# Kernel optimization log

Measured on AMD Instinct MI355X. Metric: run time of the kernel, lower is better.

The kernel has to match this reference:

```python
import jax, jax.numpy as jnp
import numpy as np

B, S, D, H = 2, 2048, 1024, 16
HD = D // H  # head dim = 64


def setup_inputs() -> dict:
    key = jax.random.key(0)
    ks = jax.random.split(key, 9)
    std = 0.02
    return {
        "hidden_states": jax.random.normal(ks[0], (B, S, D), jnp.float32),
        "wq": jax.random.normal(ks[1], (D, D), jnp.float32) * std,
        "bq": jnp.zeros((D,), jnp.float32),
        "wk": jax.random.normal(ks[2], (D, D), jnp.float32) * std,
        "bk": jnp.zeros((D,), jnp.float32),
        "wv": jax.random.normal(ks[3], (D, D), jnp.float32) * std,
        "bv": jnp.zeros((D,), jnp.float32),
        "wo": jax.random.normal(ks[4], (D, D), jnp.float32) * std,
        "bo": jnp.zeros((D,), jnp.float32),
    }


def reference(hidden_states, wq, bq, wk, bk, wv, bv, wo, bo):
    b, s, d = hidden_states.shape
    # projections (torch Linear: x @ W.T + b; here weights stored as [in,out]-equivalent transpose)
    q = hidden_states @ wq.T + bq
    k = hidden_states @ wk.T + bk
    v = hidden_states @ wv.T + bv
    # [b, h, s, hd]
    q = q.reshape(b, s, H, HD).transpose(0, 2, 1, 3)
    k = k.reshape(b, s, H, HD).transpose(0, 2, 1, 3)
    v = v.reshape(b, s, H, HD).transpose(0, 2, 1, 3)
    scores = jnp.einsum("bhqd,bhkd->bhqk", q, k) / jnp.sqrt(jnp.float32(HD))
    probs = jax.nn.softmax(scores, axis=-1)  # dropout p=0 (eval)
    ctx = jnp.einsum("bhqk,bhkd->bhqd", probs, v)
    ctx = ctx.transpose(0, 2, 1, 3).reshape(b, s, d)
    return ctx @ wo.T + bo
```

## Files before the change

### kernel.cpp

```cpp
#include <hip/hip_runtime.h>
#include <math.h>
#include <stdint.h>

constexpr int BB  = 2;
constexpr int SS  = 2048;
constexpr int DD  = 1024;
constexpr int HH  = 16;
constexpr int HDD = 64;
constexpr int MM  = BB * SS;

typedef uint16_t u16;
typedef __attribute__((ext_vector_type(4))) float    f32x4;
typedef __attribute__((ext_vector_type(8))) _Float16 f16x8;
typedef __attribute__((ext_vector_type(4))) _Float16 f16x4;
typedef __attribute__((ext_vector_type(8))) short    s16x8;
typedef __attribute__((ext_vector_type(4))) unsigned int u32x4;

__device__ __forceinline__ u16 to_f16(float f) {
    const _Float16 h = (_Float16)f;
    return __builtin_bit_cast(u16, h);
}

__device__ __forceinline__ f32x4 mfma32(s16x8 a, s16x8 b, f32x4 c) {
    return __builtin_amdgcn_mfma_f32_16x16x32_f16(
        __builtin_bit_cast(f16x8, a), __builtin_bit_cast(f16x8, b), c, 0, 0, 0);
}
__device__ __forceinline__ f32x4 mfma32_ff(s16x8 a, f16x8 b, f32x4 c) {
    return __builtin_amdgcn_mfma_f32_16x16x32_f16(
        __builtin_bit_cast(f16x8, a), b, c, 0, 0, 0);
}

__device__ __forceinline__ void load_lds16(const void* g, void* l) {
    __builtin_amdgcn_global_load_lds(
        (const __attribute__((address_space(1))) void*)g,
        (__attribute__((address_space(3))) void*)l, 16, 0, 0);
}

__global__ __launch_bounds__(256) void cast_all(
    const float* __restrict__ x,
    const float* __restrict__ w0, const float* __restrict__ w1,
    const float* __restrict__ w2, const float* __restrict__ w3,
    u16* __restrict__ xb, u16* __restrict__ wb)
{
    const int blk = blockIdx.x, tid = threadIdx.x;
    const float* src; u16* dst; int idx;
    if (blk < 2048) { src = x; dst = xb; idx = blk * 256 + tid; }
    else {
        const int b2 = blk - 2048, which = b2 >> 9;
        src = (which == 0) ? w0 : (which == 1) ? w1 : (which == 2) ? w2 : w3;
        dst = wb + ((size_t)which << 20);
        idx = (b2 & 511) * 256 + tid;
    }
    const float4* in4 = (const float4*)src;
    const float4 a = in4[idx * 2], b = in4[idx * 2 + 1];
    s16x8 v;
    v[0] = (short)to_f16(a.x); v[1] = (short)to_f16(a.y);
    v[2] = (short)to_f16(a.z); v[3] = (short)to_f16(a.w);
    v[4] = (short)to_f16(b.x); v[5] = (short)to_f16(b.y);
    v[6] = (short)to_f16(b.z); v[7] = (short)to_f16(b.w);
    *(s16x8*)(dst + (size_t)idx * 8) = v;
}

template <bool SWAP>
__device__ __forceinline__ void kloop64(
    const u16* __restrict__ Ag, const u16* __restrict__ Wg,
    u16* Abase, u16* Bbase, const int w4,
    const int lane, const int wm, const int wn, f32x4 (&acc)[4][4])
{
    const int lt = lane & 15, quad = lane >> 4;
    const int cb = w4 * 4;

#define STG64(buf_, ko_) do {                                              \
    _Pragma("unroll")                                                      \
    for (int c = 0; c < 4; ++c) {                                          \
        load_lds16(Ag + (size_t)((cb + c) * 8) * 1024 + (ko_),             \
                   Abase + (buf_) * 8192 + (cb + c) * 512);                \
        load_lds16(Wg + (size_t)((cb + c) * 8) * 1024 + (ko_),             \
                   Bbase + (buf_) * 8192 + (cb + c) * 512);                \
    } } while (0)

    STG64(0, 0);

#pragma unroll 1
    for (int it = 0; it < 8; ++it) {
        const int buf = it & 1;
        __syncthreads();
        if (it < 7) STG64(buf ^ 1, (it + 1) * 64);
        const u16* Acur = Abase + buf * 8192;
        const u16* Bcur = Bbase + buf * 8192;

        s16x8 af[2][4], bf[2][4];
#pragma unroll
        for (int kk = 0; kk < 2; ++kk) {
#pragma unroll
            for (int i = 0; i < 4; ++i) {
                const int row = wm + i * 16 + lt;
                af[kk][i] = *(const s16x8*)(Acur + row * 64 +
                                (((kk * 4 + quad) ^ (row & 7)) * 8));
            }
#pragma unroll
            for (int j = 0; j < 4; ++j) {
                const int row = wn + j * 16 + lt;
                bf[kk][j] = *(const s16x8*)(Bcur + row * 64 +
                                (((kk * 4 + quad) ^ (row & 7)) * 8));
            }
        }
#pragma unroll
        for (int i = 0; i < 4; ++i)
#pragma unroll
            for (int j = 0; j < 4; ++j) {
                if (SWAP) {
                    acc[i][j] = mfma32(bf[0][j], af[0][i], acc[i][j]);
                    acc[i][j] = mfma32(bf[1][j], af[1][i], acc[i][j]);
                } else {
                    acc[i][j] = mfma32(af[0][i], bf[0][j], acc[i][j]);
                    acc[i][j] = mfma32(af[1][i], bf[1][j], acc[i][j]);
                }
            }
    }
#undef STG64
}

template <int MODE>
__global__ __launch_bounds__(512) void gemm_mfma(
    const u16* __restrict__ A, const u16* __restrict__ Wb,
    const float* __restrict__ b0, const float* __restrict__ b1,
    const float* __restrict__ b2,
    float* __restrict__ outf, u16* __restrict__ outq, u16* __restrict__ outv)
{
    __shared__ u16 smem[65536];

    const int tid = threadIdx.x, lane = tid & 63, wid = tid >> 6;
    const int grp = wid >> 2, w4 = wid & 3;
    const int quad = lane >> 4;

    const int bm = blockIdx.y * 128;
    const int nb = blockIdx.x * 128;
    const int which = nb >> 10;
    const int ncol  = nb & 1023;
    const u16* Wblk = Wb + ((size_t)which << 20) + (size_t)ncol * 1024;

    const int rbase = lane >> 3;
    const int gu    = (lane & 7) ^ rbase;
    const u16* Ag = A    + (size_t)(bm + rbase) * 1024 + grp * 512 + gu * 8;
    const u16* Wg = Wblk + (size_t)rbase        * 1024 + grp * 512 + gu * 8;
    u16* Abase = smem + grp * 16384;
    u16* Bbase = smem + 32768 + grp * 16384;

    f32x4 acc[4][4];
#pragma unroll
    for (int i = 0; i < 4; ++i)
#pragma unroll
        for (int j = 0; j < 4; ++j) { f32x4 z = {0.f, 0.f, 0.f, 0.f}; acc[i][j] = z; }

    const int wm = (w4 >> 1) * 64, wn = (w4 & 1) * 64;
    const bool swap = (MODE == 0) || (which < 2);
    if (swap) kloop64<true >(Ag, Wg, Abase, Bbase, w4, lane, wm, wn, acc);
    else      kloop64<false>(Ag, Wg, Abase, Bbase, w4, lane, wm, wn, acc);

    __syncthreads();
    float* rp = (float*)smem;
    const int slot = (w4 * 64 + lane) * 4;
    if (grp == 1) {
#pragma unroll
        for (int i = 0; i < 4; ++i)
#pragma unroll
            for (int j = 0; j < 4; ++j)
                *(f32x4*)(rp + (i * 4 + j) * 1024 + slot) = acc[i][j];
    }
    __syncthreads();
    if (grp != 0) return;
#pragma unroll
    for (int i = 0; i < 4; ++i)
#pragma unroll
        for (int j = 0; j < 4; ++j)
            acc[i][j] += *(const f32x4*)(rp + (i * 4 + j) * 1024 + slot);

    if (MODE == 0) {
#pragma unroll
        for (int j = 0; j < 4; ++j) {
            const int n0 = nb + wn + 16 * j + quad * 4;
            const float4 bv = *(const float4*)&b0[n0];
#pragma unroll
            for (int i = 0; i < 4; ++i) {
                const int m = bm + wm + 16 * i + (lane & 15);
                f32x4 w = acc[i][j];
                w[0] += bv.x; w[1] += bv.y; w[2] += bv.z; w[3] += bv.w;
                *(f32x4*)&outf[(size_t)m * 1024 + n0] = w;
            }
        }
    } else if (which < 2) {
        const float* bias = which ? b1 : b0;
        const float scale = which ? 1.0f : 0.125f;
        u16* outb = outq + ((size_t)which << 22);
        const int h = (ncol + wn) >> 6;
#pragma unroll
        for (int j = 0; j < 4; ++j) {
            const int nl0 = ncol + wn + 16 * j + quad * 4;
            const float4 bv = *(const float4*)&bias[nl0];
            const int hd0 = 16 * j + quad * 4;
#pragma unroll
            for (int i = 0; i < 4; ++i) {
                const int m = bm + wm + 16 * i + (lane & 15);
                const int b_ = m >> 11, s = m & 2047;
                f16x4 w;
                w[0] = (_Float16)((acc[i][j][0] + bv.x) * scale);
                w[1] = (_Float16)((acc[i][j][1] + bv.y) * scale);
                w[2] = (_Float16)((acc[i][j][2] + bv.z) * scale);
                w[3] = (_Float16)((acc[i][j][3] + bv.w) * scale);
                *(f16x4*)&outb[(((size_t)(b_ * HH + h)) * SS + s) * HDD + hd0] = w;
            }
        }
    } else {
        const int kt = ((bm + wm) & 2047) >> 6;
        const int b_ = (bm + wm) >> 11;
#pragma unroll
        for (int j = 0; j < 4; ++j) {
            const int nl = ncol + wn + 16 * j + (lane & 15);
            const float bb = b2[nl];
            const int h = nl >> 6, hd = nl & 63;
            u16* vrow = outv + (((size_t)(b_ * HH + h)) * HDD + hd) * SS + kt * 64;
#pragma unroll
            for (int i = 0; i < 4; ++i) {
                const int p0 = (i >> 1) * 32 + quad * 8 + (i & 1) * 4;
                f16x4 w;
                w[0] = (_Float16)(acc[i][j][0] + bb);
                w[1] = (_Float16)(acc[i][j][1] + bb);
                w[2] = (_Float16)(acc[i][j][2] + bb);
                w[3] = (_Float16)(acc[i][j][3] + bb);
                *(f16x4*)&vrow[p0] = w;
            }
        }
    }
}

__global__ __launch_bounds__(512, 4) void attn_mfma(
    const u16* __restrict__ Q, const u16* __restrict__ Kg,
    const u16* __restrict__ Vt, u16* __restrict__ ctx)
{
    __shared__ u16 smem[32768];

    const int tid = threadIdx.x, lane = tid & 63, wid = tid >> 6;
    const int grp = wid >> 2, w4 = wid & 3;
    const int quad = lane >> 4;

    const int orig   = blockIdx.y * 16 + blockIdx.x;
    const int xcd    = orig & 7, within = orig >> 3;
    const int bh     = xcd * 4 + (within >> 4);
    const int q0     = (within & 15) * 128;

    const u16* Qb = Q  + (size_t)bh * SS * HDD;
    const u16* Kb = Kg + (size_t)bh * SS * HDD + (size_t)grp * 1024 * HDD;
    const u16* Vb = Vt + (size_t)bh * HDD * SS + grp * 1024;

    u16* Kbase = smem + grp * 8192;
    u16* Vbase = smem + 16384 + grp * 8192;

    const int qa = q0 + w4 * 32 + (lane & 15);
    const s16x8 bq0a = *(const s16x8*)(Qb + (size_t)qa * HDD + quad * 8);
    const s16x8 bq1a = *(const s16x8*)(Qb + (size_t)qa * HDD + 32 + quad * 8);
    const s16x8 bq0b = *(const s16x8*)(Qb + (size_t)(qa + 16) * HDD + quad * 8);
    const s16x8 bq1b = *(const s16x8*)(Qb + (size_t)(qa + 16) * HDD + 32 + quad * 8);

    f32x4 oa[4], ob[4];
    f32x4 la4 = {0.f, 0.f, 0.f, 0.f}, lb4 = {0.f, 0.f, 0.f, 0.f};
#pragma unroll
    for (int m = 0; m < 4; ++m) {
        f32x4 z = {0.f, 0.f, 0.f, 0.f};
        oa[m] = z; ob[m] = z;
    }
    const s16x8 ones = {15360, 15360, 15360, 15360,
                        15360, 15360, 15360, 15360};

    const int c0 = w4 * 2, c1 = c0 + 1;
    const int r0 = (c0 * 64 + lane) >> 3, lu0 = ((lane & 7) ^ (r0 & 7));
    const int r1 = (c1 * 64 + lane) >> 3, lu1 = ((lane & 7) ^ (r1 & 7));
    const u16* Kp0 = Kb + (size_t)r0 * HDD + lu0 * 8;
    const u16* Kp1 = Kb + (size_t)r1 * HDD + lu1 * 8;
    const u16* Vp0 = Vb + (size_t)r0 * SS + lu0 * 8;
    const u16* Vp1 = Vb + (size_t)r1 * SS + lu1 * 8;

    load_lds16(Kp0, Kbase + c0 * 512);
    load_lds16(Kp1, Kbase + c1 * 512);
    load_lds16(Vp0, Vbase + c0 * 512);
    load_lds16(Vp1, Vbase + c1 * 512);

    for (int kt = 0; kt < 16; ++kt) {
        const int buf = kt & 1;
        __syncthreads();

        if (kt + 1 < 16) {
            const int nb_ = (buf ^ 1) * 4096;
            load_lds16(Kp0 + (size_t)(kt + 1) * 64 * HDD, Kbase + nb_ + c0 * 512);
            load_lds16(Kp1 + (size_t)(kt + 1) * 64 * HDD, Kbase + nb_ + c1 * 512);
            load_lds16(Vp0 + (kt + 1) * 64, Vbase + nb_ + c0 * 512);
            load_lds16(Vp1 + (kt + 1) * 64, Vbase + nb_ + c1 * 512);
        }
        const u16* Kbuf = Kbase + buf * 4096;
        const u16* Vbuf = Vbase + buf * 4096;

        f32x4 Sa[4], Sb[4];
#pragma unroll
        for (int j = 0; j < 4; ++j) {
            const int row = j * 16 + (lane & 15);
            const int sw = lane & 7;
            const s16x8 ak0 = *(const s16x8*)(Kbuf + (size_t)row * 64 + ((quad    ) ^ sw) * 8);
            const s16x8 ak1 = *(const s16x8*)(Kbuf + (size_t)row * 64 + ((quad + 4) ^ sw) * 8);
            f32x4 za = {0.f, 0.f, 0.f, 0.f};
            za = mfma32(ak0, bq0a, za);
            za = mfma32(ak1, bq1a, za);
            Sa[j] = za;
            f32x4 zb = {0.f, 0.f, 0.f, 0.f};
            zb = mfma32(ak0, bq0b, zb);
            zb = mfma32(ak1, bq1b, zb);
            Sb[j] = zb;
        }

        f16x8 pb0a, pb1a, pb0b, pb1b;
        {
            u32x4 u;
            u[0] = __builtin_bit_cast(unsigned int, __builtin_amdgcn_cvt_pkrtz(__expf(Sa[0][0]), __expf(Sa[0][1])));
            u[1] = __builtin_bit_cast(unsigned int, __builtin_amdgcn_cvt_pkrtz(__expf(Sa[0][2]), __expf(Sa[0][3])));
            u[2] = __builtin_bit_cast(unsigned int, __builtin_amdgcn_cvt_pkrtz(__expf(Sa[1][0]), __expf(Sa[1][1])));
            u[3] = __builtin_bit_cast(unsigned int, __builtin_amdgcn_cvt_pkrtz(__expf(Sa[1][2]), __expf(Sa[1][3])));
            pb0a = __builtin_bit_cast(f16x8, u);
            u[0] = __builtin_bit_cast(unsigned int, __builtin_amdgcn_cvt_pkrtz(__expf(Sa[2][0]), __expf(Sa[2][1])));
            u[1] = __builtin_bit_cast(unsigned int, __builtin_amdgcn_cvt_pkrtz(__expf(Sa[2][2]), __expf(Sa[2][3])));
            u[2] = __builtin_bit_cast(unsigned int, __builtin_amdgcn_cvt_pkrtz(__expf(Sa[3][0]), __expf(Sa[3][1])));
            u[3] = __builtin_bit_cast(unsigned int, __builtin_amdgcn_cvt_pkrtz(__expf(Sa[3][2]), __expf(Sa[3][3])));
            pb1a = __builtin_bit_cast(f16x8, u);
            u[0] = __builtin_bit_cast(unsigned int, __builtin_amdgcn_cvt_pkrtz(__expf(Sb[0][0]), __expf(Sb[0][1])));
            u[1] = __builtin_bit_cast(unsigned int, __builtin_amdgcn_cvt_pkrtz(__expf(Sb[0][2]), __expf(Sb[0][3])));
            u[2] = __builtin_bit_cast(unsigned int, __builtin_amdgcn_cvt_pkrtz(__expf(Sb[1][0]), __expf(Sb[1][1])));
            u[3] = __builtin_bit_cast(unsigned int, __builtin_amdgcn_cvt_pkrtz(__expf(Sb[1][2]), __expf(Sb[1][3])));
            pb0b = __builtin_bit_cast(f16x8, u);
            u[0] = __builtin_bit_cast(unsigned int, __builtin_amdgcn_cvt_pkrtz(__expf(Sb[2][0]), __expf(Sb[2][1])));
            u[1] = __builtin_bit_cast(unsigned int, __builtin_amdgcn_cvt_pkrtz(__expf(Sb[2][2]), __expf(Sb[2][3])));
            u[2] = __builtin_bit_cast(unsigned int, __builtin_amdgcn_cvt_pkrtz(__expf(Sb[3][0]), __expf(Sb[3][1])));
            u[3] = __builtin_bit_cast(unsigned int, __builtin_amdgcn_cvt_pkrtz(__expf(Sb[3][2]), __expf(Sb[3][3])));
            pb1b = __builtin_bit_cast(f16x8, u);
        }

        la4 = mfma32_ff(ones, pb0a, la4);
        la4 = mfma32_ff(ones, pb1a, la4);
        lb4 = mfma32_ff(ones, pb0b, lb4);
        lb4 = mfma32_ff(ones, pb1b, lb4);

#pragma unroll
        for (int m = 0; m < 4; ++m) {
            const int row = m * 16 + (lane & 15);
            const int sw = lane & 7;
            const s16x8 v0 = *(const s16x8*)(Vbuf + (size_t)row * 64 + ((quad    ) ^ sw) * 8);
            const s16x8 v1 = *(const s16x8*)(Vbuf + (size_t)row * 64 + ((quad + 4) ^ sw) * 8);
            oa[m] = mfma32_ff(v0, pb0a, oa[m]);
            oa[m] = mfma32_ff(v1, pb1a, oa[m]);
            ob[m] = mfma32_ff(v0, pb0b, ob[m]);
            ob[m] = mfma32_ff(v1, pb1b, ob[m]);
        }
    }

    __syncthreads();
    float* ep = (float*)smem;
    float* lp = ep + 8 * 1088;
    if (grp == 1) {
#pragma unroll
        for (int sub = 0; sub < 2; ++sub) {
            const float* src = (sub == 0) ? (const float*)&oa[0] : (const float*)&ob[0];
            float* base = ep + (w4 * 2 + sub) * 1088 + (lane & 15) * 68 + quad * 4;
#pragma unroll
            for (int m = 0; m < 4; ++m)
                *(f32x4*)(base + m * 16) = *(const f32x4*)(src + m * 4);
        }
        if (quad == 0) {
            lp[(w4 * 2 + 0) * 16 + (lane & 15)] = la4[0];
            lp[(w4 * 2 + 1) * 16 + (lane & 15)] = lb4[0];
        }
    }
    __syncthreads();
    if (grp == 0) {
        const int b_ = bh >> 4, h = bh & 15;
#pragma unroll
        for (int sub = 0; sub < 2; ++sub) {
            const f32x4* own = (sub == 0) ? &oa[0] : &ob[0];
            const float lown = (sub == 0) ? la4[0] : lb4[0];
            const float inv = 1.f / (lown + lp[(w4 * 2 + sub) * 16 + (lane & 15)]);
            const float* base = ep + (w4 * 2 + sub) * 1088 + (lane & 15) * 68 + quad * 4;
            const int s_idx = q0 + w4 * 32 + sub * 16 + (lane & 15);
            u16* orow = ctx + ((size_t)(b_ * SS + s_idx)) * DD + h * HDD;
#pragma unroll
            for (int m = 0; m < 4; ++m) {
                const f32x4 part = *(const f32x4*)(base + m * 16);
                f16x4 w;
#pragma unroll
                for (int r = 0; r < 4; ++r)
                    w[r] = (_Float16)((own[m][r] + part[r]) * inv);
                *(f16x4*)(orow + m * 16 + quad * 4) = w;
            }
        }
    }
}

extern "C" void kernel_launch(void* const* d_in, const int* in_sizes, int n_in,
                              void* d_out, int out_size, void* d_ws, size_t ws_size,
                              hipStream_t stream)
{
    const float* x  = (const float*)d_in[0];
    const float* wq = (const float*)d_in[1];
    const float* bq = (const float*)d_in[2];
    const float* wk = (const float*)d_in[3];
    const float* bk = (const float*)d_in[4];
    const float* wv = (const float*)d_in[5];
    const float* bv = (const float*)d_in[6];
    const float* wo = (const float*)d_in[7];
    const float* bo = (const float*)d_in[8];

    u16* xb   = (u16*)d_ws;
    u16* wb   = xb  + ((size_t)4  << 20);
    u16* qk   = wb  + ((size_t)4  << 20);
    u16* vtw  = qk  + ((size_t)8  << 20);
    u16* ctxb = vtw + ((size_t)4  << 20);

    cast_all<<<4096, 256, 0, stream>>>(x, wq, wk, wv, wo, xb, wb);

    gemm_mfma<1><<<dim3(24, 32), 512, 0, stream>>>(
        xb, wb, bq, bk, bv, nullptr, qk, vtw);

    attn_mfma<<<dim3(16, 32), 512, 0, stream>>>(
        qk, qk + ((size_t)4 << 20), vtw, ctxb);

    gemm_mfma<0><<<dim3(8, 32), 512, 0, stream>>>(
        ctxb, wb + ((size_t)3 << 20), bo, nullptr, nullptr,
        (float*)d_out, nullptr, nullptr);
}
```

Baseline: 183.7 us.

## Software-pipeline attention loop: overlap QK of next tile with PV of previous

Restructures the key-tile loop so that each iteration computes QK scores and exp for tile kt while doing the PV accumulation for tile kt-1. This lets the matrix and exp work of two stages interleave instead of running back to back. V tiles move to a three-slot ring buffer in LDS so the previous tile's V stays valid while the next one loads, which raises the block's LDS use from 64KB to 80KB. Holding both the previous and the new P fragments in registers raises register pressure, and the loop is no longer unrolled.

```diff
diff --git a/kernel.cpp b/kernel.cpp
--- a/kernel.cpp
+++ b/kernel.cpp
@@ -238,7 +238,7 @@
     const u16* __restrict__ Q, const u16* __restrict__ Kg,
     const u16* __restrict__ Vt, u16* __restrict__ ctx)
 {
-    __shared__ u16 smem[32768];
+    __shared__ u16 smem[40960];
 
     const int tid = threadIdx.x, lane = tid & 63, wid = tid >> 6;
     const int grp = wid >> 2, w4 = wid & 3;
@@ -254,7 +254,7 @@
     const u16* Vb = Vt + (size_t)bh * HDD * SS + grp * 1024;
 
     u16* Kbase = smem + grp * 8192;
-    u16* Vbase = smem + 16384 + grp * 8192;
+    u16* Vbase = smem + 16384 + grp * 12288;
 
     const int qa = q0 + w4 * 32 + (lane & 15);
     const s16x8 bq0a = *(const s16x8*)(Qb + (size_t)qa * HDD + quad * 8);
@@ -280,26 +280,10 @@
     const u16* Vp0 = Vb + (size_t)r0 * SS + lu0 * 8;
     const u16* Vp1 = Vb + (size_t)r1 * SS + lu1 * 8;
 
-    load_lds16(Kp0, Kbase + c0 * 512);
-    load_lds16(Kp1, Kbase + c1 * 512);
-    load_lds16(Vp0, Vbase + c0 * 512);
-    load_lds16(Vp1, Vbase + c1 * 512);
-
-    for (int kt = 0; kt < 16; ++kt) {
-        const int buf = kt & 1;
-        __syncthreads();
-
-        if (kt + 1 < 16) {
-            const int nb_ = (buf ^ 1) * 4096;
-            load_lds16(Kp0 + (size_t)(kt + 1) * 64 * HDD, Kbase + nb_ + c0 * 512);
-            load_lds16(Kp1 + (size_t)(kt + 1) * 64 * HDD, Kbase + nb_ + c1 * 512);
-            load_lds16(Vp0 + (kt + 1) * 64, Vbase + nb_ + c0 * 512);
-            load_lds16(Vp1 + (kt + 1) * 64, Vbase + nb_ + c1 * 512);
-        }
-        const u16* Kbuf = Kbase + buf * 4096;
-        const u16* Vbuf = Vbase + buf * 4096;
-
-        f32x4 Sa[4], Sb[4];
+    f16x8 pA0, pA1, pB0, pB1;
+
+    f32x4 Sa[4], Sb[4];
+    auto qk_tiles = [&](const u16* Kbuf) {
 #pragma unroll
         for (int j = 0; j < 4; ++j) {
             const int row = j * 16 + (lane & 15);
@@ -315,49 +299,73 @@
             zb = mfma32(ak1, bq1b, zb);
             Sb[j] = zb;
         }
-
-        f16x8 pb0a, pb1a, pb0b, pb1b;
-        {
-            u32x4 u;
-            u[0] = __builtin_bit_cast(unsigned int, __builtin_amdgcn_cvt_pkrtz(__expf(Sa[0][0]), __expf(Sa[0][1])));
-            u[1] = __builtin_bit_cast(unsigned int, __builtin_amdgcn_cvt_pkrtz(__expf(Sa[0][2]), __expf(Sa[0][3])));
-            u[2] = __builtin_bit_cast(unsigned int, __builtin_amdgcn_cvt_pkrtz(__expf(Sa[1][0]), __expf(Sa[1][1])));
-            u[3] = __builtin_bit_cast(unsigned int, __builtin_amdgcn_cvt_pkrtz(__expf(Sa[1][2]), __expf(Sa[1][3])));
-            pb0a = __builtin_bit_cast(f16x8, u);
-            u[0] = __builtin_bit_cast(unsigned int, __builtin_amdgcn_cvt_pkrtz(__expf(Sa[2][0]), __expf(Sa[2][1])));
-            u[1] = __builtin_bit_cast(unsigned int, __builtin_amdgcn_cvt_pkrtz(__expf(Sa[2][2]), __expf(Sa[2][3])));
-            u[2] = __builtin_bit_cast(unsigned int, __builtin_amdgcn_cvt_pkrtz(__expf(Sa[3][0]), __expf(Sa[3][1])));
-            u[3] = __builtin_bit_cast(unsigned int, __builtin_amdgcn_cvt_pkrtz(__expf(Sa[3][2]), __expf(Sa[3][3])));
-            pb1a = __builtin_bit_cast(f16x8, u);
-            u[0] = __builtin_bit_cast(unsigned int, __builtin_amdgcn_cvt_pkrtz(__expf(Sb[0][0]), __expf(Sb[0][1])));
-            u[1] = __builtin_bit_cast(unsigned int, __builtin_amdgcn_cvt_pkrtz(__expf(Sb[0][2]), __expf(Sb[0][3])));
-            u[2] = __builtin_bit_cast(unsigned int, __builtin_amdgcn_cvt_pkrtz(__expf(Sb[1][0]), __expf(Sb[1][1])));
-            u[3] = __builtin_bit_cast(unsigned int, __builtin_amdgcn_cvt_pkrtz(__expf(Sb[1][2]), __expf(Sb[1][3])));
-            pb0b = __builtin_bit_cast(f16x8, u);
-            u[0] = __builtin_bit_cast(unsigned int, __builtin_amdgcn_cvt_pkrtz(__expf(Sb[2][0]), __expf(Sb[2][1])));
-            u[1] = __builtin_bit_cast(unsigned int, __builtin_amdgcn_cvt_pkrtz(__expf(Sb[2][2]), __expf(Sb[2][3])));
-            u[2] = __builtin_bit_cast(unsigned int, __builtin_amdgcn_cvt_pkrtz(__expf(Sb[3][0]), __expf(Sb[3][1])));
-            u[3] = __builtin_bit_cast(unsigned int, __builtin_amdgcn_cvt_pkrtz(__expf(Sb[3][2]), __expf(Sb[3][3])));
-            pb1b = __builtin_bit_cast(f16x8, u);
-        }
-
-        la4 = mfma32_ff(ones, pb0a, la4);
-        la4 = mfma32_ff(ones, pb1a, la4);
-        lb4 = mfma32_ff(ones, pb0b, lb4);
-        lb4 = mfma32_ff(ones, pb1b, lb4);
-
+    };
+    auto exp_pack = [&](const f32x4* S, f16x8& o0, f16x8& o1) {
+        u32x4 u;
+        u[0] = __builtin_bit_cast(unsigned int, __builtin_amdgcn_cvt_pkrtz(__expf(S[0][0]), __expf(S[0][1])));
+        u[1] = __builtin_bit_cast(unsigned int, __builtin_amdgcn_cvt_pkrtz(__expf(S[0][2]), __expf(S[0][3])));
+        u[2] = __builtin_bit_cast(unsigned int, __builtin_amdgcn_cvt_pkrtz(__expf(S[1][0]), __expf(S[1][1])));
+        u[3] = __builtin_bit_cast(unsigned int, __builtin_amdgcn_cvt_pkrtz(__expf(S[1][2]), __expf(S[1][3])));
+        o0 = __builtin_bit_cast(f16x8, u);
+        u[0] = __builtin_bit_cast(unsigned int, __builtin_amdgcn_cvt_pkrtz(__expf(S[2][0]), __expf(S[2][1])));
+        u[1] = __builtin_bit_cast(unsigned int, __builtin_amdgcn_cvt_pkrtz(__expf(S[2][2]), __expf(S[2][3])));
+        u[2] = __builtin_bit_cast(unsigned int, __builtin_amdgcn_cvt_pkrtz(__expf(S[3][0]), __expf(S[3][1])));
+        u[3] = __builtin_bit_cast(unsigned int, __builtin_amdgcn_cvt_pkrtz(__expf(S[3][2]), __expf(S[3][3])));
+        o1 = __builtin_bit_cast(f16x8, u);
+    };
+    auto do_pv = [&](const u16* Vbuf) {
+        la4 = mfma32_ff(ones, pA0, la4);
+        la4 = mfma32_ff(ones, pA1, la4);
+        lb4 = mfma32_ff(ones, pB0, lb4);
+        lb4 = mfma32_ff(ones, pB1, lb4);
 #pragma unroll
         for (int m = 0; m < 4; ++m) {
             const int row = m * 16 + (lane & 15);
             const int sw = lane & 7;
             const s16x8 v0 = *(const s16x8*)(Vbuf + (size_t)row * 64 + ((quad    ) ^ sw) * 8);
             const s16x8 v1 = *(const s16x8*)(Vbuf + (size_t)row * 64 + ((quad + 4) ^ sw) * 8);
-            oa[m] = mfma32_ff(v0, pb0a, oa[m]);
-            oa[m] = mfma32_ff(v1, pb1a, oa[m]);
-            ob[m] = mfma32_ff(v0, pb0b, ob[m]);
-            ob[m] = mfma32_ff(v1, pb1b, ob[m]);
-        }
-    }
+            oa[m] = mfma32_ff(v0, pA0, oa[m]);
+            oa[m] = mfma32_ff(v1, pA1, oa[m]);
+            ob[m] = mfma32_ff(v0, pB0, ob[m]);
+            ob[m] = mfma32_ff(v1, pB1, ob[m]);
+        }
+    };
+
+    load_lds16(Kp0, Kbase + c0 * 512);
+    load_lds16(Kp1, Kbase + c1 * 512);
+    load_lds16(Vp0, Vbase + c0 * 512);
+    load_lds16(Vp1, Vbase + c1 * 512);
+
+    __syncthreads();
+    load_lds16(Kp0 + 64 * HDD, Kbase + 4096 + c0 * 512);
+    load_lds16(Kp1 + 64 * HDD, Kbase + 4096 + c1 * 512);
+    load_lds16(Vp0 + 64,       Vbase + 4096 + c0 * 512);
+    load_lds16(Vp1 + 64,       Vbase + 4096 + c1 * 512);
+    qk_tiles(Kbase);
+    exp_pack(Sa, pA0, pA1);
+    exp_pack(Sb, pB0, pB1);
+
+    int sl_prev = 0, sl_next = 2;
+#pragma unroll 1
+    for (int kt = 1; kt < 16; ++kt) {
+        const int kb = kt & 1;
+        __syncthreads();
+        if (kt < 15) {
+            load_lds16(Kp0 + (size_t)(kt + 1) * 64 * HDD, Kbase + (kb ^ 1) * 4096 + c0 * 512);
+            load_lds16(Kp1 + (size_t)(kt + 1) * 64 * HDD, Kbase + (kb ^ 1) * 4096 + c1 * 512);
+            load_lds16(Vp0 + (kt + 1) * 64, Vbase + sl_next * 4096 + c0 * 512);
+            load_lds16(Vp1 + (kt + 1) * 64, Vbase + sl_next * 4096 + c1 * 512);
+        }
+        qk_tiles(Kbase + kb * 4096);
+        f16x8 nA0, nA1, nB0, nB1;
+        exp_pack(Sa, nA0, nA1);
+        exp_pack(Sb, nB0, nB1);
+        do_pv(Vbase + sl_prev * 4096);
+        pA0 = nA0; pA1 = nA1; pB0 = nB0; pB1 = nB1;
+        sl_prev = (sl_prev == 2) ? 0 : sl_prev + 1;
+        sl_next = (sl_next == 2) ? 0 : sl_next + 1;
+    }
+    do_pv(Vbase);
 
     __syncthreads();
     float* ep = (float*)smem;
```

Result: slower. 189.5 us (+3.2%).

## Process 64 query rows per wave in attention to reuse K/V tiles

Applied to the files above, without the earlier changes.

Each wave in the attention kernel now handles four 16-row query sub-tiles instead of two, so a block covers 256 queries and the grid halves. Each K and V fragment read from LDS feeds twice as many MFMAs, and each block reloads K/V half as often across the sequence. The cost is more accumulator registers, so launch bounds drop to 2 blocks per CU and the epilogue scratch grows. Fewer blocks and lower occupancy may leave CUs underused.

```diff
diff --git a/kernel.cpp b/kernel.cpp
--- a/kernel.cpp
+++ b/kernel.cpp
@@ -234,20 +234,20 @@
     }
 }
 
-__global__ __launch_bounds__(512, 4) void attn_mfma(
+__global__ __launch_bounds__(512, 2) void attn_mfma(
     const u16* __restrict__ Q, const u16* __restrict__ Kg,
     const u16* __restrict__ Vt, u16* __restrict__ ctx)
 {
-    __shared__ u16 smem[32768];
+    __shared__ u16 smem[35840];
 
     const int tid = threadIdx.x, lane = tid & 63, wid = tid >> 6;
     const int grp = wid >> 2, w4 = wid & 3;
-    const int quad = lane >> 4;
-
-    const int orig   = blockIdx.y * 16 + blockIdx.x;
+    const int quad = lane >> 4, lt = lane & 15, sw = lane & 7;
+
+    const int orig   = blockIdx.y * 8 + blockIdx.x;
     const int xcd    = orig & 7, within = orig >> 3;
-    const int bh     = xcd * 4 + (within >> 4);
-    const int q0     = (within & 15) * 128;
+    const int bh     = xcd * 4 + (within >> 3);
+    const int q0     = (within & 7) * 256;
 
     const u16* Qb = Q  + (size_t)bh * SS * HDD;
     const u16* Kb = Kg + (size_t)bh * SS * HDD + (size_t)grp * 1024 * HDD;
@@ -256,18 +256,22 @@
     u16* Kbase = smem + grp * 8192;
     u16* Vbase = smem + 16384 + grp * 8192;
 
-    const int qa = q0 + w4 * 32 + (lane & 15);
-    const s16x8 bq0a = *(const s16x8*)(Qb + (size_t)qa * HDD + quad * 8);
-    const s16x8 bq1a = *(const s16x8*)(Qb + (size_t)qa * HDD + 32 + quad * 8);
-    const s16x8 bq0b = *(const s16x8*)(Qb + (size_t)(qa + 16) * HDD + quad * 8);
-    const s16x8 bq1b = *(const s16x8*)(Qb + (size_t)(qa + 16) * HDD + 32 + quad * 8);
-
-    f32x4 oa[4], ob[4];
-    f32x4 la4 = {0.f, 0.f, 0.f, 0.f}, lb4 = {0.f, 0.f, 0.f, 0.f};
-#pragma unroll
-    for (int m = 0; m < 4; ++m) {
+    const int qa = q0 + w4 * 64 + lt;
+    s16x8 bq[4][2];
+#pragma unroll
+    for (int s = 0; s < 4; ++s) {
+        bq[s][0] = *(const s16x8*)(Qb + (size_t)(qa + 16 * s) * HDD + quad * 8);
+        bq[s][1] = *(const s16x8*)(Qb + (size_t)(qa + 16 * s) * HDD + 32 + quad * 8);
+    }
+
+    f32x4 o[4][4];
+    f32x4 l4[4];
+#pragma unroll
+    for (int s = 0; s < 4; ++s) {
         f32x4 z = {0.f, 0.f, 0.f, 0.f};
-        oa[m] = z; ob[m] = z;
+        l4[s] = z;
+#pragma unroll
+        for (int m = 0; m < 4; ++m) o[s][m] = z;
     }
     const s16x8 ones = {15360, 15360, 15360, 15360,
                         15360, 15360, 15360, 15360};
@@ -285,6 +289,7 @@
     load_lds16(Vp0, Vbase + c0 * 512);
     load_lds16(Vp1, Vbase + c1 * 512);
 
+#pragma unroll 1
     for (int kt = 0; kt < 16; ++kt) {
         const int buf = kt & 1;
         __syncthreads();
@@ -299,93 +304,78 @@
         const u16* Kbuf = Kbase + buf * 4096;
         const u16* Vbuf = Vbase + buf * 4096;
 
-        f32x4 Sa[4], Sb[4];
-#pragma unroll
-        for (int j = 0; j < 4; ++j) {
-            const int row = j * 16 + (lane & 15);
-            const int sw = lane & 7;
-            const s16x8 ak0 = *(const s16x8*)(Kbuf + (size_t)row * 64 + ((quad    ) ^ sw) * 8);
-            const s16x8 ak1 = *(const s16x8*)(Kbuf + (size_t)row * 64 + ((quad + 4) ^ sw) * 8);
-            f32x4 za = {0.f, 0.f, 0.f, 0.f};
-            za = mfma32(ak0, bq0a, za);
-            za = mfma32(ak1, bq1a, za);
-            Sa[j] = za;
-            f32x4 zb = {0.f, 0.f, 0.f, 0.f};
-            zb = mfma32(ak0, bq0b, zb);
-            zb = mfma32(ak1, bq1b, zb);
-            Sb[j] = zb;
-        }
-
-        f16x8 pb0a, pb1a, pb0b, pb1b;
-        {
-            u32x4 u;
-            u[0] = __builtin_bit_cast(unsigned int, __builtin_amdgcn_cvt_pkrtz(__expf(Sa[0][0]), __expf(Sa[0][1])));
-            u[1] = __builtin_bit_cast(unsigned int, __builtin_amdgcn_cvt_pkrtz(__expf(Sa[0][2]), __expf(Sa[0][3])));
-            u[2] = __builtin_bit_cast(unsigned int, __builtin_amdgcn_cvt_pkrtz(__expf(Sa[1][0]), __expf(Sa[1][1])));
-            u[3] = __builtin_bit_cast(unsigned int, __builtin_amdgcn_cvt_pkrtz(__expf(Sa[1][2]), __expf(Sa[1][3])));
-            pb0a = __builtin_bit_cast(f16x8, u);
-            u[0] = __builtin_bit_cast(unsigned int, __builtin_amdgcn_cvt_pkrtz(__expf(Sa[2][0]), __expf(Sa[2][1])));
-            u[1] = __builtin_bit_cast(unsigned int, __builtin_amdgcn_cvt_pkrtz(__expf(Sa[2][2]), __expf(Sa[2][3])));
-            u[2] = __builtin_bit_cast(unsigned int, __builtin_amdgcn_cvt_pkrtz(__expf(Sa[3][0]), __expf(Sa[3][1])));
-            u[3] = __builtin_bit_cast(unsigned int, __builtin_amdgcn_cvt_pkrtz(__expf(Sa[3][2]), __expf(Sa[3][3])));
-            pb1a = __builtin_bit_cast(f16x8, u);
-            u[0] = __builtin_bit_cast(unsigned int, __builtin_amdgcn_cvt_pkrtz(__expf(Sb[0][0]), __expf(Sb[0][1])));
-            u[1] = __builtin_bit_cast(unsigned int, __builtin_amdgcn_cvt_pkrtz(__expf(Sb[0][2]), __expf(Sb[0][3])));
-            u[2] = __builtin_bit_cast(unsigned int, __builtin_amdgcn_cvt_pkrtz(__expf(Sb[1][0]), __expf(Sb[1][1])));
-            u[3] = __builtin_bit_cast(unsigned int, __builtin_amdgcn_cvt_pkrtz(__expf(Sb[1][2]), __expf(Sb[1][3])));
-            pb0b = __builtin_bit_cast(f16x8, u);
-            u[0] = __builtin_bit_cast(unsigned int, __builtin_amdgcn_cvt_pkrtz(__expf(Sb[2][0]), __expf(Sb[2][1])));
-            u[1] = __builtin_bit_cast(unsigned int, __builtin_amdgcn_cvt_pkrtz(__expf(Sb[2][2]), __expf(Sb[2][3])));
-            u[2] = __builtin_bit_cast(unsigned int, __builtin_amdgcn_cvt_pkrtz(__expf(Sb[3][0]), __expf(Sb[3][1])));
-            u[3] = __builtin_bit_cast(unsigned int, __builtin_amdgcn_cvt_pkrtz(__expf(Sb[3][2]), __expf(Sb[3][3])));
-            pb1b = __builtin_bit_cast(f16x8, u);
-        }
-
-        la4 = mfma32_ff(ones, pb0a, la4);
-        la4 = mfma32_ff(ones, pb1a, la4);
-        lb4 = mfma32_ff(ones, pb0b, lb4);
-        lb4 = mfma32_ff(ones, pb1b, lb4);
+        f16x8 P[4][2];
+#pragma unroll
+        for (int h = 0; h < 2; ++h) {
+            f32x4 S[4][2];
+#pragma unroll
+            for (int j = 0; j < 2; ++j) {
+                const int row = (h * 2 + j) * 16 + lt;
+                const s16x8 ak0 = *(const s16x8*)(Kbuf + (size_t)row * 64 + ((quad    ) ^ sw) * 8);
+                const s16x8 ak1 = *(const s16x8*)(Kbuf + (size_t)row * 64 + ((quad + 4) ^ sw) * 8);
+#pragma unroll
+                for (int s = 0; s < 4; ++s) {
+                    f32x4 z = {0.f, 0.f, 0.f, 0.f};
+                    z = mfma32(ak0, bq[s][0], z);
+                    z = mfma32(ak1, bq[s][1], z);
+                    S[s][j] = z;
+                }
+            }
+#pragma unroll
+            for (int s = 0; s < 4; ++s) {
+                u32x4 u;
+                u[0] = __builtin_bit_cast(unsigned int, __builtin_amdgcn_cvt_pkrtz(__expf(S[s][0][0]), __expf(S[s][0][1])));
+                u[1] = __builtin_bit_cast(unsigned int, __builtin_amdgcn_cvt_pkrtz(__expf(S[s][0][2]), __expf(S[s][0][3])));
+                u[2] = __builtin_bit_cast(unsigned int, __builtin_amdgcn_cvt_pkrtz(__expf(S[s][1][0]), __expf(S[s][1][1])));
+                u[3] = __builtin_bit_cast(unsigned int, __builtin_amdgcn_cvt_pkrtz(__expf(S[s][1][2]), __expf(S[s][1][3])));
+                P[s][h] = __builtin_bit_cast(f16x8, u);
+            }
+        }
+
+#pragma unroll
+        for (int s = 0; s < 4; ++s) {
+            l4[s] = mfma32_ff(ones, P[s][0], l4[s]);
+            l4[s] = mfma32_ff(ones, P[s][1], l4[s]);
+        }
 
 #pragma unroll
         for (int m = 0; m < 4; ++m) {
-            const int row = m * 16 + (lane & 15);
-            const int sw = lane & 7;
+            const int row = m * 16 + lt;
             const s16x8 v0 = *(const s16x8*)(Vbuf + (size_t)row * 64 + ((quad    ) ^ sw) * 8);
             const s16x8 v1 = *(const s16x8*)(Vbuf + (size_t)row * 64 + ((quad + 4) ^ sw) * 8);
-            oa[m] = mfma32_ff(v0, pb0a, oa[m]);
-            oa[m] = mfma32_ff(v1, pb1a, oa[m]);
-            ob[m] = mfma32_ff(v0, pb0b, ob[m]);
-            ob[m] = mfma32_ff(v1, pb1b, ob[m]);
+#pragma unroll
+            for (int s = 0; s < 4; ++s) {
+                o[s][m] = mfma32_ff(v0, P[s][0], o[s][m]);
+                o[s][m] = mfma32_ff(v1, P[s][1], o[s][m]);
+            }
         }
     }
 
     __syncthreads();
     float* ep = (float*)smem;
-    float* lp = ep + 8 * 1088;
+    float* lp = ep + 16 * 1088;
     if (grp == 1) {
 #pragma unroll
-        for (int sub = 0; sub < 2; ++sub) {
-            const float* src = (sub == 0) ? (const float*)&oa[0] : (const float*)&ob[0];
-            float* base = ep + (w4 * 2 + sub) * 1088 + (lane & 15) * 68 + quad * 4;
+        for (int s = 0; s < 4; ++s) {
+            float* base = ep + (w4 * 4 + s) * 1088 + lt * 68 + quad * 4;
 #pragma unroll
             for (int m = 0; m < 4; ++m)
-                *(f32x4*)(base + m * 16) = *(const f32x4*)(src + m * 4);
+                *(f32x4*)(base + m * 16) = o[s][m];
         }
         if (quad == 0) {
-            lp[(w4 * 2 + 0) * 16 + (lane & 15)] = la4[0];
-            lp[(w4 * 2 + 1) * 16 + (lane & 15)] = lb4[0];
+#pragma unroll
+            for (int s = 0; s < 4; ++s)
+                lp[(w4 * 4 + s) * 16 + lt] = l4[s][0];
         }
     }
     __syncthreads();
     if (grp == 0) {
         const int b_ = bh >> 4, h = bh & 15;
 #pragma unroll
-        for (int sub = 0; sub < 2; ++sub) {
-            const f32x4* own = (sub == 0) ? &oa[0] : &ob[0];
-            const float lown = (sub == 0) ? la4[0] : lb4[0];
-            const float inv = 1.f / (lown + lp[(w4 * 2 + sub) * 16 + (lane & 15)]);
-            const float* base = ep + (w4 * 2 + sub) * 1088 + (lane & 15) * 68 + quad * 4;
-            const int s_idx = q0 + w4 * 32 + sub * 16 + (lane & 15);
+        for (int s = 0; s < 4; ++s) {
+            const float inv = 1.f / (l4[s][0] + lp[(w4 * 4 + s) * 16 + lt]);
+            const float* base = ep + (w4 * 4 + s) * 1088 + lt * 68 + quad * 4;
+            const int s_idx = q0 + w4 * 64 + s * 16 + lt;
             u16* orow = ctx + ((size_t)(b_ * SS + s_idx)) * DD + h * HDD;
 #pragma unroll
             for (int m = 0; m < 4; ++m) {
@@ -393,7 +383,7 @@
                 f16x4 w;
 #pragma unroll
                 for (int r = 0; r < 4; ++r)
-                    w[r] = (_Float16)((own[m][r] + part[r]) * inv);
+                    w[r] = (_Float16)((o[s][m][r] + part[r]) * inv);
                 *(f16x4*)(orow + m * 16 + quad * 4) = w;
             }
         }
@@ -425,7 +415,7 @@
     gemm_mfma<1><<<dim3(24, 32), 512, 0, stream>>>(
         xb, wb, bq, bk, bv, nullptr, qk, vtw);
 
-    attn_mfma<<<dim3(16, 32), 512, 0, stream>>>(
+    attn_mfma<<<dim3(8, 32), 512, 0, stream>>>(
         qk, qk + ((size_t)4 << 20), vtw, ctxb);
 
     gemm_mfma<0><<<dim3(8, 32), 512, 0, stream>>>(
```

Measured after the change: 179.3 us (median of 3 runs). 2.4% less time.
